# Kernel optimization log

Measured on AMD Instinct MI355X. Metric: run time of the kernel, lower is better.

## Reference

```python
import jax, jax.numpy as jnp
import numpy as np

N_NODES = 100000
N_EDGES = 800000
DIM = 128
BN_EPS = 1e-5


def setup_inputs() -> dict:
    key = jax.random.key(0)
    k1, k2, k3 = jax.random.split(key, 3)
    x = jax.random.normal(k1, (N_NODES, DIM), dtype=jnp.float32)
    edge_index = jax.random.randint(k2, (2, N_EDGES), 0, N_NODES, dtype=jnp.int64)
    # xavier-uniform-like init for the linear weight [out, in]
    limit = float(np.sqrt(6.0 / (DIM + DIM)))
    W = jax.random.uniform(k3, (DIM, DIM), dtype=jnp.float32, minval=-limit, maxval=limit)
    bias = jnp.zeros((DIM,), dtype=jnp.float32)
    bn_gamma = jnp.ones((DIM,), dtype=jnp.float32)
    bn_beta = jnp.zeros((DIM,), dtype=jnp.float32)
    return {"x": x, "edge_index": edge_index, "W": W, "bias": bias,
            "bn_gamma": bn_gamma, "bn_beta": bn_beta, "bit_sum": 0}


def reference(x, edge_index, W, bias, bn_gamma, bn_beta, bit_sum):
    n = x.shape[0]
    # Linear (no bias), is_q=False path; q_xw treated as identity.
    h = x @ W.T                                   # [N, D]
    row, col = edge_index[0], edge_index[1]
    # symmetric degree normalization: deg computed over destination (col)
    deg = jax.ops.segment_sum(jnp.ones_like(col, dtype=h.dtype), col, num_segments=n)
    deg_inv_sqrt = jnp.where(deg > 0, jax.lax.rsqrt(jnp.maximum(deg, 1.0)), 0.0)
    norm = deg_inv_sqrt[row] * deg_inv_sqrt[col]  # [E]
    # message: norm * x_j (x_j = h[row]), aggregate (add) at col
    msg = norm[:, None] * h[row]                  # [E, D]
    out = jax.ops.segment_sum(msg, col, num_segments=n)  # [N, D]
    out = out + bias
    # BatchNorm1d (training mode: batch stats, biased variance)
    mean = jnp.mean(out, axis=0)
    var = jnp.var(out, axis=0)
    out = (out - mean) * jax.lax.rsqrt(var + BN_EPS) * bn_gamma + bn_beta
    # activation
    out = jax.nn.relu(out)
    # residual (in_dim == out_dim); dropout p=0 -> identity
    out = out + x
    return (out, 0)
```

## Files before the change

kernel.cpp:

```cpp
#include <hip/hip_runtime.h>
#include <cstddef>

#define NN 100000
#define DD 128
#define ND (NN * DD)
#define BN_EPS 1e-5f
#define LDA 136
#define NREP 16
#define NBKT 98
#define EPB 4096

typedef __bf16 bf16_t;
typedef bf16_t bf16x8 __attribute__((ext_vector_type(8)));
typedef float f32x4 __attribute__((ext_vector_type(4)));
typedef unsigned int uint;
typedef unsigned short ushort;


__device__ __forceinline__ ushort f2b(float f) {
    uint u = __builtin_bit_cast(uint, f);
    u += 0x7FFFu + ((u >> 16) & 1u);
    return (ushort)(u >> 16);
}
__device__ __forceinline__ float b2f(uint s) {
    return __builtin_bit_cast(float, s << 16);
}

__device__ __forceinline__ int detect_i64(const int* __restrict__ ei) {
    __shared__ int sflag;
    int t = threadIdx.x;
    if (t < 64) {
        int hi = ei[2 * t + 1];
        unsigned long long b = __ballot(hi == 0);
        if (t == 0) sflag = (b == ~0ull) ? 1 : 0;
    }
    __syncthreads();
    return sflag;
}

__global__ __launch_bounds__(256) void k_prep(const int* __restrict__ ei,
                                              int* __restrict__ bktot, int E, int nbh,
                                              const float* __restrict__ x,
                                              uint* __restrict__ xb,
                                              const float* __restrict__ W,
                                              uint* __restrict__ wb) {
    if ((int)blockIdx.x < nbh) {
        int f = detect_i64(ei);
        __shared__ int hist[NBKT];
        int t = threadIdx.x;
        if (t < NBKT) hist[t] = 0;
        __syncthreads();
        int base = blockIdx.x * EPB;
        int count = min(EPB, E - base);
        for (int i = t; i < count; i += 256) {
            int e = base + i;
            int c = f ? ei[2 * (E + e)] : ei[E + e];
            atomicAdd(&hist[c >> 10], 1);
        }
        __syncthreads();
        if (t < NBKT && hist[t] > 0) atomicAdd(&bktot[t], hist[t]);
        return;
    }
    int i = (blockIdx.x - nbh) * 256 + threadIdx.x;
    const float* src;
    uint* dst;
    int j;
    if (i < ND / 8) { src = x; dst = xb; j = i; }
    else { j = i - ND / 8; if (j >= (DD * DD) / 8) return; src = W; dst = wb; }
    const float4* s4 = (const float4*)src;
    float4 a = s4[2 * j], b = s4[2 * j + 1];
    uint4 o;
    o.x = (uint)f2b(a.x) | ((uint)f2b(a.y) << 16);
    o.y = (uint)f2b(a.z) | ((uint)f2b(a.w) << 16);
    o.z = (uint)f2b(b.x) | ((uint)f2b(b.y) << 16);
    o.w = (uint)f2b(b.z) | ((uint)f2b(b.w) << 16);
    ((uint4*)dst)[j] = o;
}

__global__ __launch_bounds__(256) void k_bin(const int* __restrict__ ei,
                                             const int* __restrict__ bktot,
                                             int* __restrict__ bcur,
                                             uint2* __restrict__ pairs, int E) {
    int f = detect_i64(ei);
    __shared__ int bb[NBKT], hist[NBKT], scur[NBKT];
    int t = threadIdx.x;
    if (t < NBKT) { bb[t] = bktot[t]; hist[t] = 0; }
    __syncthreads();
    if (t == 0) {
        int run = 0;
        for (int i = 0; i < NBKT; ++i) { int v = bb[i]; bb[i] = run; run += v; }
    }
    int base = blockIdx.x * EPB;
    int count = min(EPB, E - base);
    int rr[16], cc[16];
#pragma unroll
    for (int k = 0; k < 16; ++k) {
        int i = t + k * 256;
        if (i < count) {
            int e = base + i;
            int r, c;
            if (f) { r = ei[2 * e]; c = ei[2 * (E + e)]; }
            else   { r = ei[e];     c = ei[E + e]; }
            rr[k] = r; cc[k] = c;
            atomicAdd(&hist[c >> 10], 1);
        }
    }
    __syncthreads();
    if (t < NBKT) scur[t] = bb[t] + atomicAdd(&bcur[t], hist[t]);
    __syncthreads();
#pragma unroll
    for (int k = 0; k < 16; ++k) {
        int i = t + k * 256;
        if (i < count) {
            int b = cc[k] >> 10;
            int pos = atomicAdd(&scur[b], 1);
            pairs[pos] = (uint2){(uint)rr[k], (uint)cc[k]};
        }
    }
}

__global__ __launch_bounds__(256) void k_cnt(const uint2* __restrict__ pairs,
                                             const int* __restrict__ bktot,
                                             int* __restrict__ ptr0,
                                             int* __restrict__ cnt,
                                             float* __restrict__ dinv,
                                             int* __restrict__ srow) {
    __shared__ int hist[1024];
    __shared__ int scur[1024];
    __shared__ int ls[256];
    __shared__ int bb[NBKT];
    __shared__ int se0, se1;
    int b = blockIdx.x;
    int t = threadIdx.x;
    if (t < NBKT) bb[t] = bktot[t];
#pragma unroll
    for (int i = 0; i < 4; ++i) hist[t + i * 256] = 0;
    __syncthreads();
    if (t == 0) {
        int run = 0;
        for (int i = 0; i < b; ++i) run += bb[i];
        se0 = run; se1 = run + bb[b];
    }
    __syncthreads();
    int e0 = se0, e1 = se1;
    int nodebase = b << 10;
    for (int i = e0 + t; i < e1; i += 256)
        atomicAdd(&hist[(int)pairs[i].y - nodebase], 1);
    __syncthreads();
    int c4[4];
    int lsum = 0;
#pragma unroll
    for (int i = 0; i < 4; ++i) { c4[i] = hist[t * 4 + i]; lsum += c4[i]; }
    ls[t] = lsum;
    __syncthreads();
    for (int o = 1; o < 256; o <<= 1) {
        int v = (t >= o) ? ls[t - o] : 0;
        __syncthreads();
        ls[t] += v;
        __syncthreads();
    }
    int run = ls[t] - lsum + e0;
#pragma unroll
    for (int i = 0; i < 4; ++i) {
        int idx = nodebase + t * 4 + i;
        if (idx < NN) {
            ptr0[idx] = run;
            cnt[idx] = c4[i];
            dinv[idx] = c4[i] > 0 ? rsqrtf((float)c4[i]) : 0.f;
        }
        scur[t * 4 + i] = run;
        run += c4[i];
    }
    __syncthreads();
    for (int i = e0 + t; i < e1; i += 256) {
        uint2 p = pairs[i];
        int pos = atomicAdd(&scur[(int)p.y - nodebase], 1);
        srow[pos] = (int)p.x;
    }
}

__global__ __launch_bounds__(256, 4) void k_gg(const uint* __restrict__ xb,
                                               const int* __restrict__ srow,
                                               const int* __restrict__ ptr0,
                                               const int* __restrict__ cnt,
                                               const float* __restrict__ dinv,
                                               const ushort* __restrict__ wb,
                                               ushort* __restrict__ hb,
                                               float* __restrict__ csr,
                                               float* __restrict__ cqr) {
    __shared__ ushort sA[64 * LDA];
    __shared__ float cp[4][128], cq[4][128];
    int t = threadIdx.x;
    int wave = t >> 6, lane = t & 63;
    size_t rowbase = (size_t)blockIdx.x * 64;

    int mn = (int)rowbase + wave * 16 + (lane & 15);
    int sv = 0, kv = 0;
    float dv = 0.f;
    if (lane < 16 && mn < NN) { sv = ptr0[mn]; kv = cnt[mn]; dv = dinv[mn]; }
    for (int i = 0; i < 16; ++i) {
        int s = __shfl(sv, i);
        int k = __shfl(kv, i);
        float dc = __shfl(dv, i);
        float ax = 0.f, ay = 0.f;
        for (int base = 0; base < k; base += 64) {
            int m = min(k - base, 64);
            int rj = 0; float wj = 0.f;
            if (lane < m) { rj = srow[s + base + lane]; wj = dinv[rj]; }
            int j = 0;
            for (; j + 8 <= m; j += 8) {
                int r0 = __shfl(rj, j);     float w0 = __shfl(wj, j);
                int r1 = __shfl(rj, j + 1); float w1 = __shfl(wj, j + 1);
                int r2 = __shfl(rj, j + 2); float w2 = __shfl(wj, j + 2);
                int r3 = __shfl(rj, j + 3); float w3 = __shfl(wj, j + 3);
                int r4 = __shfl(rj, j + 4); float w4 = __shfl(wj, j + 4);
                int r5 = __shfl(rj, j + 5); float w5 = __shfl(wj, j + 5);
                int r6 = __shfl(rj, j + 6); float w6 = __shfl(wj, j + 6);
                int r7 = __shfl(rj, j + 7); float w7 = __shfl(wj, j + 7);
                uint v0 = xb[(size_t)r0 * 64 + lane];
                uint v1 = xb[(size_t)r1 * 64 + lane];
                uint v2 = xb[(size_t)r2 * 64 + lane];
                uint v3 = xb[(size_t)r3 * 64 + lane];
                uint v4 = xb[(size_t)r4 * 64 + lane];
                uint v5 = xb[(size_t)r5 * 64 + lane];
                uint v6 = xb[(size_t)r6 * 64 + lane];
                uint v7 = xb[(size_t)r7 * 64 + lane];
                ax = fmaf(w0, b2f(v0 & 0xFFFFu), ax); ay = fmaf(w0, b2f(v0 >> 16), ay);
                ax = fmaf(w1, b2f(v1 & 0xFFFFu), ax); ay = fmaf(w1, b2f(v1 >> 16), ay);
                ax = fmaf(w2, b2f(v2 & 0xFFFFu), ax); ay = fmaf(w2, b2f(v2 >> 16), ay);
                ax = fmaf(w3, b2f(v3 & 0xFFFFu), ax); ay = fmaf(w3, b2f(v3 >> 16), ay);
                ax = fmaf(w4, b2f(v4 & 0xFFFFu), ax); ay = fmaf(w4, b2f(v4 >> 16), ay);
                ax = fmaf(w5, b2f(v5 & 0xFFFFu), ax); ay = fmaf(w5, b2f(v5 >> 16), ay);
                ax = fmaf(w6, b2f(v6 & 0xFFFFu), ax); ay = fmaf(w6, b2f(v6 >> 16), ay);
                ax = fmaf(w7, b2f(v7 & 0xFFFFu), ax); ay = fmaf(w7, b2f(v7 >> 16), ay);
            }
            for (; j + 4 <= m; j += 4) {
                int r0 = __shfl(rj, j);     float w0 = __shfl(wj, j);
                int r1 = __shfl(rj, j + 1); float w1 = __shfl(wj, j + 1);
                int r2 = __shfl(rj, j + 2); float w2 = __shfl(wj, j + 2);
                int r3 = __shfl(rj, j + 3); float w3 = __shfl(wj, j + 3);
                uint v0 = xb[(size_t)r0 * 64 + lane];
                uint v1 = xb[(size_t)r1 * 64 + lane];
                uint v2 = xb[(size_t)r2 * 64 + lane];
                uint v3 = xb[(size_t)r3 * 64 + lane];
                ax = fmaf(w0, b2f(v0 & 0xFFFFu), ax); ay = fmaf(w0, b2f(v0 >> 16), ay);
                ax = fmaf(w1, b2f(v1 & 0xFFFFu), ax); ay = fmaf(w1, b2f(v1 >> 16), ay);
                ax = fmaf(w2, b2f(v2 & 0xFFFFu), ax); ay = fmaf(w2, b2f(v2 >> 16), ay);
                ax = fmaf(w3, b2f(v3 & 0xFFFFu), ax); ay = fmaf(w3, b2f(v3 >> 16), ay);
            }
            for (; j < m; ++j) {
                int r = __shfl(rj, j);
                float w = __shfl(wj, j);
                uint v = xb[(size_t)r * 64 + lane];
                ax = fmaf(w, b2f(v & 0xFFFFu), ax);
                ay = fmaf(w, b2f(v >> 16), ay);
            }
        }
        uint o = (uint)f2b(dc * ax) | ((uint)f2b(dc * ay) << 16);
        *(uint*)(sA + (wave * 16 + i) * LDA + lane * 2) = o;
    }
    __syncthreads();

    int quad = lane >> 4, l16 = lane & 15;
    bf16x8 Af[4];
#pragma unroll
    for (int ks = 0; ks < 4; ++ks)
        Af[ks] = __builtin_bit_cast(
            bf16x8, *(const uint4*)(sA + (wave * 16 + l16) * LDA + ks * 32 + quad * 8));

#pragma unroll
    for (int ct = 0; ct < 8; ++ct) {
        bf16x8 Bf[4];
#pragma unroll
        for (int ks = 0; ks < 4; ++ks)
            Bf[ks] = __builtin_bit_cast(
                bf16x8,
                *(const uint4*)(wb + (size_t)(ct * 16 + l16) * 128 + ks * 32 + quad * 8));
        f32x4 acc = (f32x4){0.f, 0.f, 0.f, 0.f};
#pragma unroll
        for (int ks = 0; ks < 4; ++ks)
            acc = __builtin_amdgcn_mfma_f32_16x16x32_bf16(Af[ks], Bf[ks], acc, 0, 0, 0);
        float ss = 0.f, qq = 0.f;
#pragma unroll
        for (int r = 0; r < 4; ++r) {
            float v = acc[r];
            ss += v; qq += v * v;
            size_t row = rowbase + wave * 16 + quad * 4 + r;
            if (row < NN) hb[row * 128 + ct * 16 + l16] = f2b(v);
        }
        ss += __shfl_xor(ss, 16); ss += __shfl_xor(ss, 32);
        qq += __shfl_xor(qq, 16); qq += __shfl_xor(qq, 32);
        if (quad == 0) { cp[wave][ct * 16 + l16] = ss; cq[wave][ct * 16 + l16] = qq; }
    }
    __syncthreads();
    if (t < 128) {
        int rep = (blockIdx.x & (NREP - 1)) * 128 + t;
        atomicAdd(&csr[rep], cp[0][t] + cp[1][t] + cp[2][t] + cp[3][t]);
        atomicAdd(&cqr[rep], cq[0][t] + cq[1][t] + cq[2][t] + cq[3][t]);
    }
}

__global__ __launch_bounds__(256) void k_final(const uint* __restrict__ hb,
                                               const uint* __restrict__ xb,
                                               const float* __restrict__ gamma,
                                               const float* __restrict__ beta,
                                               const float* __restrict__ csr,
                                               const float* __restrict__ cqr,
                                               float* __restrict__ out, int out_size) {
    __shared__ float sa[128], sb[128];
    int t = threadIdx.x;
    const float invN = 1.0f / NN;
    if (t < 128) {
        float s = 0.f;
        for (int i = 0; i < NREP; ++i) s += csr[i * 128 + t];
        sa[t] = s * invN;
    } else {
        int c = t - 128;
        float s = 0.f;
        for (int i = 0; i < NREP; ++i) s += cqr[i * 128 + c];
        sb[c] = s * invN;
    }
    __syncthreads();
    if (t < 128) {
        float m = sa[t];
        float var = sb[t] - m * m;
        float inv = rsqrtf(var + BN_EPS);
        float A = inv * gamma[t];
        float B = beta[t] - m * A;
        sa[t] = A; sb[t] = B;
    }
    __syncthreads();

    int c0 = (t & 7) * 16;
    int u8 = blockIdx.x * 512 + t * 2;
    uint4 hv0 = ((const uint4*)hb)[u8], hv1 = ((const uint4*)hb)[u8 + 1];
    uint4 xv0 = ((const uint4*)xb)[u8], xv1 = ((const uint4*)xb)[u8 + 1];
    uint hu[8] = {hv0.x, hv0.y, hv0.z, hv0.w, hv1.x, hv1.y, hv1.z, hv1.w};
    uint xu[8] = {xv0.x, xv0.y, xv0.z, xv0.w, xv1.x, xv1.y, xv1.z, xv1.w};
    float res[16];
#pragma unroll
    for (int p = 0; p < 8; ++p) {
        int c = c0 + p * 2;
        float h0 = b2f(hu[p] & 0xFFFFu), h1 = b2f(hu[p] >> 16);
        float x0 = b2f(xu[p] & 0xFFFFu), x1 = b2f(xu[p] >> 16);
        res[2 * p]     = fmaxf(fmaf(h0, sa[c],     sb[c]),     0.f) + x0;
        res[2 * p + 1] = fmaxf(fmaf(h1, sa[c + 1], sb[c + 1]), 0.f) + x1;
    }
    float4* o4 = (float4*)out;
    int ob = blockIdx.x * 1024 + t * 4;
#pragma unroll
    for (int q = 0; q < 4; ++q)
        o4[ob + q] = (float4){res[4 * q], res[4 * q + 1], res[4 * q + 2], res[4 * q + 3]};
    if (blockIdx.x == 0 && t == 0 && out_size > ND) out[ND] = 0.0f;
}

extern "C" void kernel_launch(void* const* d_in, const int* in_sizes, int n_in,
                              void* d_out, int out_size, void* d_ws, size_t ws_size,
                              hipStream_t stream) {
    const float* x     = (const float*)d_in[0];
    const int*   ei    = (const int*)d_in[1];
    const float* W     = (const float*)d_in[2];
    const float* gamma = (const float*)d_in[4];
    const float* beta  = (const float*)d_in[5];
    float* ws = (float*)d_ws;
    float* out = (float*)d_out;

    uint*   hb       = (uint*)ws;
    uint*   xb       = hb + ND / 2;
    float*  csr      = (float*)(xb + ND / 2);
    float*  cqr      = csr + NREP * 128;
    int*    bktot    = (int*)(cqr + NREP * 128);
    int*    bcur     = bktot + 128;
    int*    cnt      = bcur + 128;
    int*    ptr0     = cnt + NN;
    float*  dinv     = (float*)(ptr0 + NN);
    int*    srow     = (int*)(dinv + NN);

    int E = in_sizes[1] / 2;
    uint* wb = (uint*)(srow + E);

    uint2* pairs = (uint2*)hb;

    int nbc = (ND / 8 + (DD * DD) / 8 + 255) / 256;
    int nbin = (E + EPB - 1) / EPB;

    hipMemsetAsync(csr, 0, (size_t)(2 * NREP * 128 + 256) * 4, stream);
    k_prep<<<nbin + nbc, 256, 0, stream>>>(ei, bktot, E, nbin, x, xb, W, wb);
    k_bin<<<nbin, 256, 0, stream>>>(ei, bktot, bcur, pairs, E);
    k_cnt<<<NBKT, 256, 0, stream>>>(pairs, bktot, ptr0, cnt, dinv, srow);
    k_gg<<<(NN + 63) / 64, 256, 0, stream>>>(xb, srow, ptr0, cnt, dinv,
                                             (const ushort*)wb, (ushort*)hb, csr, cqr);
    k_final<<<ND / 4096, 256, 0, stream>>>(hb, xb, gamma, beta, csr, cqr,
                                           out, out_size);
}
```

Before: 230.8 us.

## Interleave gathers for two destination nodes per wave and alias LDS buffers

The gather-aggregate loop in k_gg now walks the neighbour lists of two destination rows at once. It issues eight independent row loads per step instead of one node's, to expose more memory-level parallelism. Neighbour weights are now loaded per edge from dinv rather than shuffled, and tail edges are masked with zero weights instead of handled in remainder loops. The BN partial-sum scratch (cp/cq) now reuses the sA shared buffer behind an extra barrier, which lowers LDS footprint. The cost is some wasted loads when the two degrees differ, plus more scalar loads of dinv.

```diff
diff --git a/kernel.cpp b/kernel.cpp
--- a/kernel.cpp
+++ b/kernel.cpp
@@ -188,8 +188,8 @@
                                                ushort* __restrict__ hb,
                                                float* __restrict__ csr,
                                                float* __restrict__ cqr) {
-    __shared__ ushort sA[64 * LDA];
-    __shared__ float cp[4][128], cq[4][128];
+    __shared__ char smem[64 * LDA * 2];
+    ushort* sAp = (ushort*)smem;
     int t = threadIdx.x;
     int wave = t >> 6, lane = t & 63;
     size_t rowbase = (size_t)blockIdx.x * 64;
@@ -198,66 +198,55 @@
     int sv = 0, kv = 0;
     float dv = 0.f;
     if (lane < 16 && mn < NN) { sv = ptr0[mn]; kv = cnt[mn]; dv = dinv[mn]; }
-    for (int i = 0; i < 16; ++i) {
-        int s = __shfl(sv, i);
-        int k = __shfl(kv, i);
-        float dc = __shfl(dv, i);
-        float ax = 0.f, ay = 0.f;
-        for (int base = 0; base < k; base += 64) {
-            int m = min(k - base, 64);
-            int rj = 0; float wj = 0.f;
-            if (lane < m) { rj = srow[s + base + lane]; wj = dinv[rj]; }
-            int j = 0;
-            for (; j + 8 <= m; j += 8) {
-                int r0 = __shfl(rj, j);     float w0 = __shfl(wj, j);
-                int r1 = __shfl(rj, j + 1); float w1 = __shfl(wj, j + 1);
-                int r2 = __shfl(rj, j + 2); float w2 = __shfl(wj, j + 2);
-                int r3 = __shfl(rj, j + 3); float w3 = __shfl(wj, j + 3);
-                int r4 = __shfl(rj, j + 4); float w4 = __shfl(wj, j + 4);
-                int r5 = __shfl(rj, j + 5); float w5 = __shfl(wj, j + 5);
-                int r6 = __shfl(rj, j + 6); float w6 = __shfl(wj, j + 6);
-                int r7 = __shfl(rj, j + 7); float w7 = __shfl(wj, j + 7);
-                uint v0 = xb[(size_t)r0 * 64 + lane];
-                uint v1 = xb[(size_t)r1 * 64 + lane];
-                uint v2 = xb[(size_t)r2 * 64 + lane];
-                uint v3 = xb[(size_t)r3 * 64 + lane];
-                uint v4 = xb[(size_t)r4 * 64 + lane];
-                uint v5 = xb[(size_t)r5 * 64 + lane];
-                uint v6 = xb[(size_t)r6 * 64 + lane];
-                uint v7 = xb[(size_t)r7 * 64 + lane];
-                ax = fmaf(w0, b2f(v0 & 0xFFFFu), ax); ay = fmaf(w0, b2f(v0 >> 16), ay);
-                ax = fmaf(w1, b2f(v1 & 0xFFFFu), ax); ay = fmaf(w1, b2f(v1 >> 16), ay);
-                ax = fmaf(w2, b2f(v2 & 0xFFFFu), ax); ay = fmaf(w2, b2f(v2 >> 16), ay);
-                ax = fmaf(w3, b2f(v3 & 0xFFFFu), ax); ay = fmaf(w3, b2f(v3 >> 16), ay);
-                ax = fmaf(w4, b2f(v4 & 0xFFFFu), ax); ay = fmaf(w4, b2f(v4 >> 16), ay);
-                ax = fmaf(w5, b2f(v5 & 0xFFFFu), ax); ay = fmaf(w5, b2f(v5 >> 16), ay);
-                ax = fmaf(w6, b2f(v6 & 0xFFFFu), ax); ay = fmaf(w6, b2f(v6 >> 16), ay);
-                ax = fmaf(w7, b2f(v7 & 0xFFFFu), ax); ay = fmaf(w7, b2f(v7 >> 16), ay);
+
+    for (int i = 0; i < 16; i += 2) {
+        int sa0 = __shfl(sv, i),     kA = __shfl(kv, i);
+        int sb0 = __shfl(sv, i + 1), kB = __shfl(kv, i + 1);
+        float dA = __shfl(dv, i), dB = __shfl(dv, i + 1);
+        float axA = 0.f, ayA = 0.f, axB = 0.f, ayB = 0.f;
+        int kmax = max(kA, kB);
+        for (int base = 0; base < kmax; base += 64) {
+            int mA = kA - base; mA = mA > 64 ? 64 : mA;
+            int mB = kB - base; mB = mB > 64 ? 64 : mB;
+            int rjA = 0, rjB = 0;
+            if (lane < mA) rjA = srow[sa0 + base + lane];
+            if (lane < mB) rjB = srow[sb0 + base + lane];
+            int mm = max(mA, mB);
+            for (int j = 0; j < mm; j += 4) {
+                int ra0 = __shfl(rjA, j),     rb0 = __shfl(rjB, j);
+                int ra1 = __shfl(rjA, j + 1), rb1 = __shfl(rjB, j + 1);
+                int ra2 = __shfl(rjA, j + 2), rb2 = __shfl(rjB, j + 2);
+                int ra3 = __shfl(rjA, j + 3), rb3 = __shfl(rjB, j + 3);
+                uint va0 = xb[(size_t)ra0 * 64 + lane];
+                uint vb0 = xb[(size_t)rb0 * 64 + lane];
+                uint va1 = xb[(size_t)ra1 * 64 + lane];
+                uint vb1 = xb[(size_t)rb1 * 64 + lane];
+                uint va2 = xb[(size_t)ra2 * 64 + lane];
+                uint vb2 = xb[(size_t)rb2 * 64 + lane];
+                uint va3 = xb[(size_t)ra3 * 64 + lane];
+                uint vb3 = xb[(size_t)rb3 * 64 + lane];
+                float wa0 = dinv[ra0], wbb0 = dinv[rb0];
+                float wa1 = dinv[ra1], wbb1 = dinv[rb1];
+                float wa2 = dinv[ra2], wbb2 = dinv[rb2];
+                float wa3 = dinv[ra3], wbb3 = dinv[rb3];
+                wa0 = (j     < mA) ? wa0 : 0.f;  wbb0 = (j     < mB) ? wbb0 : 0.f;
+                wa1 = (j + 1 < mA) ? wa1 : 0.f;  wbb1 = (j + 1 < mB) ? wbb1 : 0.f;
+                wa2 = (j + 2 < mA) ? wa2 : 0.f;  wbb2 = (j + 2 < mB) ? wbb2 : 0.f;
+                wa3 = (j + 3 < mA) ? wa3 : 0.f;  wbb3 = (j + 3 < mB) ? wbb3 : 0.f;
+                axA = fmaf(wa0, b2f(va0 & 0xFFFFu), axA); ayA = fmaf(wa0, b2f(va0 >> 16), ayA);
+                axA = fmaf(wa1, b2f(va1 & 0xFFFFu), axA); ayA = fmaf(wa1, b2f(va1 >> 16), ayA);
+                axA = fmaf(wa2, b2f(va2 & 0xFFFFu), axA); ayA = fmaf(wa2, b2f(va2 >> 16), ayA);
+                axA = fmaf(wa3, b2f(va3 & 0xFFFFu), axA); ayA = fmaf(wa3, b2f(va3 >> 16), ayA);
+                axB = fmaf(wbb0, b2f(vb0 & 0xFFFFu), axB); ayB = fmaf(wbb0, b2f(vb0 >> 16), ayB);
+                axB = fmaf(wbb1, b2f(vb1 & 0xFFFFu), axB); ayB = fmaf(wbb1, b2f(vb1 >> 16), ayB);
+                axB = fmaf(wbb2, b2f(vb2 & 0xFFFFu), axB); ayB = fmaf(wbb2, b2f(vb2 >> 16), ayB);
+                axB = fmaf(wbb3, b2f(vb3 & 0xFFFFu), axB); ayB = fmaf(wbb3, b2f(vb3 >> 16), ayB);
             }
-            for (; j + 4 <= m; j += 4) {
-                int r0 = __shfl(rj, j);     float w0 = __shfl(wj, j);
-                int r1 = __shfl(rj, j + 1); float w1 = __shfl(wj, j + 1);
-                int r2 = __shfl(rj, j + 2); float w2 = __shfl(wj, j + 2);
-                int r3 = __shfl(rj, j + 3); float w3 = __shfl(wj, j + 3);
-                uint v0 = xb[(size_t)r0 * 64 + lane];
-                uint v1 = xb[(size_t)r1 * 64 + lane];
-                uint v2 = xb[(size_t)r2 * 64 + lane];
-                uint v3 = xb[(size_t)r3 * 64 + lane];
-                ax = fmaf(w0, b2f(v0 & 0xFFFFu), ax); ay = fmaf(w0, b2f(v0 >> 16), ay);
-                ax = fmaf(w1, b2f(v1 & 0xFFFFu), ax); ay = fmaf(w1, b2f(v1 >> 16), ay);
-                ax = fmaf(w2, b2f(v2 & 0xFFFFu), ax); ay = fmaf(w2, b2f(v2 >> 16), ay);
-                ax = fmaf(w3, b2f(v3 & 0xFFFFu), ax); ay = fmaf(w3, b2f(v3 >> 16), ay);
-            }
-            for (; j < m; ++j) {
-                int r = __shfl(rj, j);
-                float w = __shfl(wj, j);
-                uint v = xb[(size_t)r * 64 + lane];
-                ax = fmaf(w, b2f(v & 0xFFFFu), ax);
-                ay = fmaf(w, b2f(v >> 16), ay);
-            }
-        }
-        uint o = (uint)f2b(dc * ax) | ((uint)f2b(dc * ay) << 16);
-        *(uint*)(sA + (wave * 16 + i) * LDA + lane * 2) = o;
+        }
+        *(uint*)(sAp + (wave * 16 + i) * LDA + lane * 2) =
+            (uint)f2b(dA * axA) | ((uint)f2b(dA * ayA) << 16);
+        *(uint*)(sAp + (wave * 16 + i + 1) * LDA + lane * 2) =
+            (uint)f2b(dB * axB) | ((uint)f2b(dB * ayB) << 16);
     }
     __syncthreads();
 
@@ -266,7 +255,10 @@
 #pragma unroll
     for (int ks = 0; ks < 4; ++ks)
         Af[ks] = __builtin_bit_cast(
-            bf16x8, *(const uint4*)(sA + (wave * 16 + l16) * LDA + ks * 32 + quad * 8));
+            bf16x8, *(const uint4*)(sAp + (wave * 16 + l16) * LDA + ks * 32 + quad * 8));
+    __syncthreads();
+    float (*cp)[128] = (float (*)[128])smem;
+    float (*cq)[128] = (float (*)[128])(smem + 4 * 128 * 4);
 
 #pragma unroll
     for (int ct = 0; ct < 8; ++ct) {
```

After: 231.2 us. About the same (+0.2%).
